# Kernel optimization log

Hardware: AMD Instinct MI355X
Metric: run time of the kernel (lower is better)

The kernel has to match this reference:

```python
import jax, jax.numpy as jnp
import numpy as np

H = 128  # hidden_dim
D = 128  # input_dim


def _lstm_scan(x_seq, Wih, Whh, bih, bhh, reverse=False):
    """x_seq: [T,B,Din]; returns h outputs [T,B,H] in original time order.
    PyTorch LSTMCell gate order: i, f, g, o."""
    hdim = Whh.shape[1]
    B = x_seq.shape[1]
    # Precompute input projections for all timesteps in one GEMM.
    xg = jnp.einsum('tbd,gd->tbg', x_seq, Wih) + bih  # [T,B,4H]

    def step(carry, xg_t):
        h, c = carry
        gates = xg_t + h @ Whh.T + bhh
        i, f, g, o = jnp.split(gates, 4, axis=-1)
        i = jax.nn.sigmoid(i)
        f = jax.nn.sigmoid(f)
        g = jnp.tanh(g)
        o = jax.nn.sigmoid(o)
        c = f * c + i * g
        h = o * jnp.tanh(c)
        return (h, c), h

    h0 = jnp.zeros((B, hdim), dtype=x_seq.dtype)
    c0 = jnp.zeros((B, hdim), dtype=x_seq.dtype)
    _, hs = jax.lax.scan(step, (h0, c0), xg, reverse=reverse)
    return hs  # [T,B,H], original time order (scan reverse handles bw dir)


def _bilstm_layer(x_seq, params_fw, params_bw):
    fw = _lstm_scan(x_seq, *params_fw, reverse=False)
    bw = _lstm_scan(x_seq, *params_bw, reverse=True)
    return jnp.concatenate([fw, bw], axis=-1)  # [T,B,2H]


def _make_cell_params(key, in_dim, hid):
    k1, k2, k3, k4 = jax.random.split(key, 4)
    s = 1.0 / np.sqrt(hid)
    return (
        jax.random.uniform(k1, (4 * hid, in_dim), jnp.float32, -s, s),
        jax.random.uniform(k2, (4 * hid, hid), jnp.float32, -s, s),
        jax.random.uniform(k3, (4 * hid,), jnp.float32, -s, s),
        jax.random.uniform(k4, (4 * hid,), jnp.float32, -s, s),
    )


def setup_inputs() -> dict:
    key = jax.random.key(0)
    ks = jax.random.split(key, 6)
    B, T = 64, 1024
    x = jax.random.normal(ks[0], (B, T, D), jnp.float32)
    lengths = jax.random.randint(ks[1], (B,), 1, T + 1, jnp.int64 if jax.config.jax_enable_x64 else jnp.int32)
    inp = {'x': x, 'lengths': lengths}
    names = ['fw1', 'bw1', 'fw2', 'bw2']
    in_dims = [D, D, 2 * H, 2 * H]
    for name, idim, k in zip(names, in_dims, ks[2:]):
        Wih, Whh, bih, bhh = _make_cell_params(k, idim, H)
        inp[f'Wih_{name}'] = Wih
        inp[f'Whh_{name}'] = Whh
        inp[f'bih_{name}'] = bih
        inp[f'bhh_{name}'] = bhh
    return inp


def reference(x, lengths,
              Wih_fw1, Whh_fw1, bih_fw1, bhh_fw1,
              Wih_bw1, Whh_bw1, bih_bw1, bhh_bw1,
              Wih_fw2, Whh_fw2, bih_fw2, bhh_fw2,
              Wih_bw2, Whh_bw2, bih_bw2, bhh_bw2):
    # lengths is unused in the original forward as well.
    xt = jnp.transpose(x, (1, 0, 2))  # [T,B,D] time-major for scan
    out1 = _bilstm_layer(xt,
                         (Wih_fw1, Whh_fw1, bih_fw1, bhh_fw1),
                         (Wih_bw1, Whh_bw1, bih_bw1, bhh_bw1))
    out2 = _bilstm_layer(out1,
                         (Wih_fw2, Whh_fw2, bih_fw2, bhh_fw2),
                         (Wih_bw2, Whh_bw2, bih_bw2, bhh_bw2))
    return jnp.transpose(out2, (1, 0, 2))  # [B,T,2H]
```

## Files before the change

### kernel.cpp

```cpp
#include <hip/hip_runtime.h>
#include <hip/hip_fp16.h>
#include <stdint.h>


#define T_SEQ 1024
#define B_SZ  64
#define M_TOT 65536

typedef _Float16 h2_t __attribute__((ext_vector_type(2)));
typedef _Float16 f16x8 __attribute__((ext_vector_type(8)));
typedef float f32x4 __attribute__((ext_vector_type(4)));

__device__ inline uint32_t pack2(float a, float b) {
  uint16_t ua = __builtin_bit_cast(uint16_t, (_Float16)a);
  uint16_t ub = __builtin_bit_cast(uint16_t, (_Float16)b);
  return (uint32_t)ua | ((uint32_t)ub << 16);
}

template <int CTRL>
__device__ inline float dppf(float v) {
  return __builtin_bit_cast(
      float, __builtin_amdgcn_update_dpp(0, __builtin_bit_cast(int, v), CTRL,
                                         0xF, 0xF, true));
}


__global__ void prep_whB(const float* __restrict__ Whh, uint32_t* __restrict__ dst) {
  int idx = blockIdx.x * 256 + threadIdx.x;
  int R = idx >> 6, kw = idx & 63;
  int w = R >> 7, nt = (R >> 4) & 7, cc = R & 15;
  int j = 32 * w + 8 * (nt >> 1) + 2 * (cc >> 2) + (nt & 1);
  int g = (cc & 3) * 128 + j;
  dst[idx] = pack2(Whh[g * 128 + 2 * kw], Whh[g * 128 + 2 * kw + 1]);
}

template <int KW>
__global__ void prep_bt(const float* __restrict__ Wih, uint32_t* __restrict__ dst) {
  int idx = blockIdx.x * 256 + threadIdx.x;
  constexpr int SH = (KW == 64) ? 6 : 7;
  int g = idx >> SH, kw = idx & (KW - 1);
  dst[idx] = pack2(Wih[g * (2 * KW) + 2 * kw], Wih[g * (2 * KW) + 2 * kw + 1]);
}

__global__ void prep_biasc(const float* __restrict__ bih, const float* __restrict__ bhh,
                           float* __restrict__ dst) {
  int idx = blockIdx.x * 256 + threadIdx.x;
  if (idx < 512) dst[idx] = bih[idx] + bhh[idx];
}

__global__ void prep_x(const float2* __restrict__ x2, uint32_t* __restrict__ xf16) {
  int idx = blockIdx.x * 256 + threadIdx.x;
  float2 v = x2[idx];
  xf16[idx] = pack2(v.x, v.y);
}

template <int KW>
__global__ __launch_bounds__(256) void xg_gemm(
    const uint32_t* __restrict__ A, const uint32_t* __restrict__ Bt,
    const float* __restrict__ biascat, uint16_t* __restrict__ xg) {
  const int n0 = blockIdx.x * 64;
  const int m0 = blockIdx.y * 64;
  const int tid = threadIdx.x;
  __shared__ uint32_t At[64][36];
  __shared__ uint32_t Bts[64][36];
  const int lr = tid >> 2, lq = tid & 3;
  const int wave = tid >> 6, lane = tid & 63;
  const int wm = wave >> 1, wn = wave & 1;
  const int q = lane >> 4, ln16 = lane & 15;
  f32x4 acc[2][2] = {};
  for (int kb = 0; kb < KW; kb += 16) {
    uint4 av = *(const uint4*)&A[(size_t)(m0 + lr) * KW + kb + lq * 4];
    uint4 bv = *(const uint4*)&Bt[(size_t)(n0 + lr) * KW + kb + lq * 4];
    __syncthreads();
    *(uint4*)&At[lr][lq * 4] = av;
    *(uint4*)&Bts[lr][lq * 4] = bv;
    __syncthreads();
#pragma unroll
    for (int mi = 0; mi < 2; mi++) {
      f16x8 af = *(const f16x8*)&At[wm * 32 + mi * 16 + ln16][q * 4];
#pragma unroll
      for (int ni = 0; ni < 2; ni++) {
        f16x8 bf = *(const f16x8*)&Bts[wn * 32 + ni * 16 + ln16][q * 4];
        acc[mi][ni] = __builtin_amdgcn_mfma_f32_16x16x32_f16(af, bf, acc[mi][ni], 0, 0, 0);
      }
    }
  }
#pragma unroll
  for (int mi = 0; mi < 2; mi++)
#pragma unroll
    for (int ni = 0; ni < 2; ni++) {
      int n = n0 + wn * 32 + ni * 16 + ln16;
      int cell = n >> 9, g = n & 511;
      int j = g & 127, pg = g >> 7;
      int PI = ((j >> 5) << 7) | (((j >> 3) & 3) << 5) | (((j >> 1) & 3) << 3) |
               (pg << 1) | (j & 1);
      float bs = biascat[n];
#pragma unroll
      for (int i = 0; i < 4; i++) {
        int m = m0 + wm * 32 + mi * 16 + q * 4 + i;
        float v = acc[mi][ni][i] + bs;
        xg[((size_t)cell * M_TOT + m) * 512 + PI] =
            __builtin_bit_cast(uint16_t, (_Float16)v);
      }
    }
}

template <bool FINAL>
__global__ __launch_bounds__(256, 1) void scan_kernel(
    const uint16_t* __restrict__ xg, const uint32_t* __restrict__ whB,
    uint32_t* __restrict__ hout, float* __restrict__ fout) {
  const int tid = threadIdx.x;
  const int w = tid >> 6;
  const int lane = tid & 63;
  const int q = lane >> 4;
  const int ln16 = lane & 15;
  const int mq = ln16 >> 2;
  const int p = ln16 & 3;
  const int b = blockIdx.x & 63;
  const int dir = blockIdx.x >> 6;

  __shared__ __align__(16) uint32_t hbuf[2][64];

  f16x8 wb[8][4];
  {
    const uint32_t* wp = whB + (size_t)dir * 512 * 64;
#pragma unroll
    for (int nt = 0; nt < 8; nt++)
#pragma unroll
      for (int kt = 0; kt < 4; kt++)
        wb[nt][kt] = *(const f16x8*)&wp[(128 * w + 16 * nt + ln16) * 64 + 16 * kt + 4 * q];
  }
#pragma unroll
  for (int nt = 0; nt < 8; nt++)
#pragma unroll
    for (int kt = 0; kt < 4; kt++) asm volatile("" : "+v"(wb[nt][kt]));

  const float kmul = (p == 2) ? (-2.0f * 1.44269504f) : -1.44269504f;
  const float gm = (p == 2) ? 2.0f : 1.0f;
  const float gb = (p == 2) ? -1.0f : 0.0f;

  const uint32_t* xgp = (const uint32_t*)xg + ((size_t)dir * M_TOT + (size_t)b * T_SEQ) * 256 + tid;

  if (tid < 64) hbuf[0][tid] = 0u;
  float c0 = 0.0f, c1 = 0.0f;
  const f32x4 zero4 = {0.0f, 0.0f, 0.0f, 0.0f};

  uint32_t xr[8];
#pragma unroll
  for (int k = 0; k < 4; k++) {
    const int tk = dir ? (T_SEQ - 1 - k) : k;
    xr[k] = xgp[(size_t)tk * 256];
  }
  __syncthreads();

  for (int s0 = 0; s0 < T_SEQ; s0 += 8) {
#pragma unroll
    for (int nt = 0; nt < 8; nt++)
#pragma unroll
      for (int kt = 0; kt < 4; kt++) asm volatile("" : "+v"(wb[nt][kt]));
#pragma unroll
    for (int k = 0; k < 8; k++) {
      const int s = s0 + k;
      const int par = k & 1;

      {
        int sn = s + 4;
        sn = (sn < T_SEQ) ? sn : (T_SEQ - 1);
        const int tn = dir ? (T_SEQ - 1 - sn) : sn;
        xr[(k + 4) & 7] = xgp[(size_t)tn * 256];
      }

      const uint4* hb4 = (const uint4*)&hbuf[par][0];
      f32x4 acc[8];
      {
        f16x8 hk = __builtin_bit_cast(f16x8, hb4[q]);
#pragma unroll
        for (int nt = 0; nt < 8; nt++)
          acc[nt] = __builtin_amdgcn_mfma_f32_16x16x32_f16(hk, wb[nt][0], zero4, 0, 0, 0);
      }
#pragma unroll
      for (int kt = 1; kt < 4; kt++) {
        f16x8 hk = __builtin_bit_cast(f16x8, hb4[kt * 4 + q]);
#pragma unroll
        for (int nt = 0; nt < 8; nt++)
          acc[nt] = __builtin_amdgcn_mfma_f32_16x16x32_f16(hk, wb[nt][kt], acc[nt], 0, 0, 0);
      }

      float z0 = (q & 2) ? ((q & 1) ? acc[6][0] : acc[4][0])
                         : ((q & 1) ? acc[2][0] : acc[0][0]);
      float z1 = (q & 2) ? ((q & 1) ? acc[7][0] : acc[5][0])
                         : ((q & 1) ? acc[3][0] : acc[1][0]);

      h2_t xv = __builtin_bit_cast(h2_t, xr[k]);
      z0 += (float)xv[0];
      z1 += (float)xv[1];

      float e0 = __builtin_amdgcn_exp2f(z0 * kmul);
      float e1 = __builtin_amdgcn_exp2f(z1 * kmul);
      float sg0 = __builtin_amdgcn_rcpf(1.0f + e0);
      float sg1 = __builtin_amdgcn_rcpf(1.0f + e1);
      float gv0 = __builtin_fmaf(sg0, gm, gb);
      float gv1 = __builtin_fmaf(sg1, gm, gb);

      float gi0 = dppf<0x00>(gv0), gf0 = dppf<0x55>(gv0);
      float gg0 = dppf<0xAA>(gv0), go0 = dppf<0xFF>(gv0);
      float gi1 = dppf<0x00>(gv1), gf1 = dppf<0x55>(gv1);
      float gg1 = dppf<0xAA>(gv1), go1 = dppf<0xFF>(gv1);

      c0 = __builtin_fmaf(gf0, c0, gi0 * gg0);
      c1 = __builtin_fmaf(gf1, c1, gi1 * gg1);
      float ec0 = __builtin_amdgcn_exp2f(c0 * (-2.0f * 1.44269504f));
      float ec1 = __builtin_amdgcn_exp2f(c1 * (-2.0f * 1.44269504f));
      float th0 = __builtin_fmaf(2.0f, __builtin_amdgcn_rcpf(1.0f + ec0), -1.0f);
      float th1 = __builtin_fmaf(2.0f, __builtin_amdgcn_rcpf(1.0f + ec1), -1.0f);
      float h0 = go0 * th0;
      float h1 = go1 * th1;

      if (p == 0) {
        const int uo = 16 * w + 4 * q + mq;
        uint32_t hu = pack2(h0, h1);
        hbuf[par ^ 1][uo] = hu;
        const int t = dir ? (T_SEQ - 1 - s) : s;
        if (FINAL) {
          float2 hv = {h0, h1};
          ((float2*)fout)[(size_t)(b * T_SEQ + t) * 128 + dir * 64 + uo] = hv;
        } else {
          hout[(size_t)(b * T_SEQ + t) * 128 + dir * 64 + uo] = hu;
        }
      }
      asm volatile("s_waitcnt lgkmcnt(0)" ::: "memory");
      __builtin_amdgcn_s_barrier();
      asm volatile("" ::: "memory");
    }
  }
}

extern "C" void kernel_launch(void* const* d_in, const int* in_sizes, int n_in,
                              void* d_out, int out_size, void* d_ws, size_t ws_size,
                              hipStream_t stream) {
  const float* x = (const float*)d_in[0];
  const float* Wih_fw1 = (const float*)d_in[2];
  const float* Whh_fw1 = (const float*)d_in[3];
  const float* bih_fw1 = (const float*)d_in[4];
  const float* bhh_fw1 = (const float*)d_in[5];
  const float* Wih_bw1 = (const float*)d_in[6];
  const float* Whh_bw1 = (const float*)d_in[7];
  const float* bih_bw1 = (const float*)d_in[8];
  const float* bhh_bw1 = (const float*)d_in[9];
  const float* Wih_fw2 = (const float*)d_in[10];
  const float* Whh_fw2 = (const float*)d_in[11];
  const float* bih_fw2 = (const float*)d_in[12];
  const float* bhh_fw2 = (const float*)d_in[13];
  const float* Wih_bw2 = (const float*)d_in[14];
  const float* Whh_bw2 = (const float*)d_in[15];
  const float* bih_bw2 = (const float*)d_in[16];
  const float* bhh_bw2 = (const float*)d_in[17];

  uint8_t* ws = (uint8_t*)d_ws;
  uint32_t* whbuf = (uint32_t*)(ws + 0);
  uint32_t* btbuf1 = (uint32_t*)(ws + 524288);
  uint32_t* btbuf2 = (uint32_t*)(ws + 786432);
  float* biascat = (float*)(ws + 1310720);
  uint32_t* xf16 = (uint32_t*)(ws + 2097152);
  uint32_t* out1 = (uint32_t*)(ws + 18874368);
  uint16_t* xgbuf = (uint16_t*)(ws + 52428800);
  float* fout = (float*)d_out;

  prep_whB<<<128, 256, 0, stream>>>(Whh_fw1, whbuf + 0 * 32768);
  prep_whB<<<128, 256, 0, stream>>>(Whh_bw1, whbuf + 1 * 32768);
  prep_whB<<<128, 256, 0, stream>>>(Whh_fw2, whbuf + 2 * 32768);
  prep_whB<<<128, 256, 0, stream>>>(Whh_bw2, whbuf + 3 * 32768);
  prep_bt<64><<<128, 256, 0, stream>>>(Wih_fw1, btbuf1 + 0);
  prep_bt<64><<<128, 256, 0, stream>>>(Wih_bw1, btbuf1 + 512 * 64);
  prep_bt<128><<<256, 256, 0, stream>>>(Wih_fw2, btbuf2 + 0);
  prep_bt<128><<<256, 256, 0, stream>>>(Wih_bw2, btbuf2 + 512 * 128);
  prep_biasc<<<2, 256, 0, stream>>>(bih_fw1, bhh_fw1, biascat + 0);
  prep_biasc<<<2, 256, 0, stream>>>(bih_bw1, bhh_bw1, biascat + 512);
  prep_biasc<<<2, 256, 0, stream>>>(bih_fw2, bhh_fw2, biascat + 1024);
  prep_biasc<<<2, 256, 0, stream>>>(bih_bw2, bhh_bw2, biascat + 1536);
  prep_x<<<(B_SZ * T_SEQ * 64) / 256, 256, 0, stream>>>((const float2*)x, xf16);

  xg_gemm<64><<<dim3(16, 1024), 256, 0, stream>>>(xf16, btbuf1, biascat, xgbuf);
  scan_kernel<false><<<128, 256, 0, stream>>>(xgbuf, whbuf + 0, out1, nullptr);

  xg_gemm<128><<<dim3(16, 1024), 256, 0, stream>>>(out1, btbuf2, biascat + 1024, xgbuf);
  scan_kernel<true><<<128, 256, 0, stream>>>(xgbuf, whbuf + 2 * 32768, nullptr, fout);
}
```

Before: 1.327 ms.

## Split recurrent matvec between MFMA and packed dot2 VALU per step

The per-step h·Whh product in the scan kernel is split: half of the hidden units (64) are computed with MFMA as before, and the other half with v_dot2 fp16 instructions from register-resident weights, followed by DPP cross-lane reductions. The aim is to shorten the serial latency of each recurrent step by halving the MFMA chain and running the other half on the VALU at the same time. Weight prep, the xg permutation and the hidden-state layout (now 16-bit per unit, outputs written as two separate halves) are all changed to match. The trade-offs are higher register pressure from 64 extra weight words per thread and extra VALU and DPP work on the critical path.

```diff
diff --git a/kernel.cpp b/kernel.cpp
--- a/kernel.cpp
+++ b/kernel.cpp
@@ -10,6 +10,11 @@
 typedef _Float16 h2_t __attribute__((ext_vector_type(2)));
 typedef _Float16 f16x8 __attribute__((ext_vector_type(8)));
 typedef float f32x4 __attribute__((ext_vector_type(4)));
+
+__device__ inline float dot2(uint32_t a, uint32_t b, float c) {
+  return __builtin_amdgcn_fdot2(__builtin_bit_cast(h2_t, a),
+                                __builtin_bit_cast(h2_t, b), c, false);
+}
 
 __device__ inline uint32_t pack2(float a, float b) {
   uint16_t ua = __builtin_bit_cast(uint16_t, (_Float16)a);
@@ -25,12 +30,18 @@
 }
 
 
-__global__ void prep_whB(const float* __restrict__ Whh, uint32_t* __restrict__ dst) {
+__global__ void prep_whBM(const float* __restrict__ Whh, uint32_t* __restrict__ dst) {
   int idx = blockIdx.x * 256 + threadIdx.x;
   int R = idx >> 6, kw = idx & 63;
-  int w = R >> 7, nt = (R >> 4) & 7, cc = R & 15;
-  int j = 32 * w + 8 * (nt >> 1) + 2 * (cc >> 2) + (nt & 1);
-  int g = (cc & 3) * 128 + j;
+  int w = R >> 6, nt = (R >> 4) & 3, cc = R & 15;
+  int g = (cc & 3) * 128 + 16 * w + 4 * nt + (cc >> 2);
+  dst[idx] = pack2(Whh[g * 128 + 2 * kw], Whh[g * 128 + 2 * kw + 1]);
+}
+
+__global__ void prep_whV(const float* __restrict__ Whh, uint32_t* __restrict__ dst) {
+  int idx = blockIdx.x * 256 + threadIdx.x;
+  int kw = idx >> 8, c2 = idx & 255;
+  int g = (c2 & 3) * 128 + 64 + (c2 >> 2);
   dst[idx] = pack2(Whh[g * 128 + 2 * kw], Whh[g * 128 + 2 * kw + 1]);
 }
 
@@ -92,8 +103,14 @@
       int n = n0 + wn * 32 + ni * 16 + ln16;
       int cell = n >> 9, g = n & 511;
       int j = g & 127, pg = g >> 7;
-      int PI = ((j >> 5) << 7) | (((j >> 3) & 3) << 5) | (((j >> 1) & 3) << 3) |
-               (pg << 1) | (j & 1);
+      int PI;
+      if (j < 64) {
+        int tidm = 64 * (j >> 4) + 16 * ((j >> 2) & 3) + 4 * (j & 3) + pg;
+        PI = tidm << 1;
+      } else {
+        int tidv = 4 * (j - 64) + pg;
+        PI = (tidv << 1) | 1;
+      }
       float bs = biascat[n];
 #pragma unroll
       for (int i = 0; i < 4; i++) {
@@ -107,8 +124,8 @@
 
 template <bool FINAL>
 __global__ __launch_bounds__(256, 1) void scan_kernel(
-    const uint16_t* __restrict__ xg, const uint32_t* __restrict__ whB,
-    uint32_t* __restrict__ hout, float* __restrict__ fout) {
+    const uint16_t* __restrict__ xg, const uint32_t* __restrict__ whc,
+    uint16_t* __restrict__ hout, float* __restrict__ fout) {
   const int tid = threadIdx.x;
   const int w = tid >> 6;
   const int lane = tid & 63;
@@ -116,24 +133,36 @@
   const int ln16 = lane & 15;
   const int mq = ln16 >> 2;
   const int p = ln16 & 3;
+  const int uq = tid >> 2;
   const int b = blockIdx.x & 63;
   const int dir = blockIdx.x >> 6;
 
-  __shared__ __align__(16) uint32_t hbuf[2][64];
-
-  f16x8 wb[8][4];
+  __shared__ __align__(16) uint16_t hbuf[2][128];
+
+  f16x8 wb[4][4];
+  uint32_t wq[4][16];
   {
-    const uint32_t* wp = whB + (size_t)dir * 512 * 64;
-#pragma unroll
-    for (int nt = 0; nt < 8; nt++)
+    const uint32_t* wpm = whc + (size_t)dir * 32768;
+    const uint32_t* wpv = wpm + 16384;
+#pragma unroll
+    for (int nt = 0; nt < 4; nt++)
 #pragma unroll
       for (int kt = 0; kt < 4; kt++)
-        wb[nt][kt] = *(const f16x8*)&wp[(128 * w + 16 * nt + ln16) * 64 + 16 * kt + 4 * q];
+        wb[nt][kt] = *(const f16x8*)&wpm[(64 * w + 16 * nt + ln16) * 64 + 16 * kt + 4 * q];
+#pragma unroll
+    for (int r = 0; r < 4; r++)
+#pragma unroll
+      for (int w2 = 0; w2 < 16; w2++)
+        wq[r][w2] = wpv[(16 * p + w2) * 256 + 4 * uq + r];
   }
 #pragma unroll
-  for (int nt = 0; nt < 8; nt++)
+  for (int nt = 0; nt < 4; nt++)
 #pragma unroll
     for (int kt = 0; kt < 4; kt++) asm volatile("" : "+v"(wb[nt][kt]));
+#pragma unroll
+  for (int r = 0; r < 4; r++)
+#pragma unroll
+    for (int w2 = 0; w2 < 16; w2++) asm volatile("" : "+v"(wq[r][w2]));
 
   const float kmul = (p == 2) ? (-2.0f * 1.44269504f) : -1.44269504f;
   const float gm = (p == 2) ? 2.0f : 1.0f;
@@ -141,7 +170,7 @@
 
   const uint32_t* xgp = (const uint32_t*)xg + ((size_t)dir * M_TOT + (size_t)b * T_SEQ) * 256 + tid;
 
-  if (tid < 64) hbuf[0][tid] = 0u;
+  if (tid < 128) hbuf[0][tid] = (uint16_t)0;
   float c0 = 0.0f, c1 = 0.0f;
   const f32x4 zero4 = {0.0f, 0.0f, 0.0f, 0.0f};
 
@@ -155,9 +184,13 @@
 
   for (int s0 = 0; s0 < T_SEQ; s0 += 8) {
 #pragma unroll
-    for (int nt = 0; nt < 8; nt++)
+    for (int nt = 0; nt < 4; nt++)
 #pragma unroll
       for (int kt = 0; kt < 4; kt++) asm volatile("" : "+v"(wb[nt][kt]));
+#pragma unroll
+    for (int r = 0; r < 4; r++)
+#pragma unroll
+      for (int w2 = 0; w2 < 16; w2++) asm volatile("" : "+v"(wq[r][w2]));
 #pragma unroll
     for (int k = 0; k < 8; k++) {
       const int s = s0 + k;
@@ -171,29 +204,59 @@
       }
 
       const uint4* hb4 = (const uint4*)&hbuf[par][0];
-      f32x4 acc[8];
+      f32x4 acc[4];
       {
         f16x8 hk = __builtin_bit_cast(f16x8, hb4[q]);
 #pragma unroll
-        for (int nt = 0; nt < 8; nt++)
+        for (int nt = 0; nt < 4; nt++)
           acc[nt] = __builtin_amdgcn_mfma_f32_16x16x32_f16(hk, wb[nt][0], zero4, 0, 0, 0);
       }
 #pragma unroll
       for (int kt = 1; kt < 4; kt++) {
         f16x8 hk = __builtin_bit_cast(f16x8, hb4[kt * 4 + q]);
 #pragma unroll
-        for (int nt = 0; nt < 8; nt++)
+        for (int nt = 0; nt < 4; nt++)
           acc[nt] = __builtin_amdgcn_mfma_f32_16x16x32_f16(hk, wb[nt][kt], acc[nt], 0, 0, 0);
       }
 
-      float z0 = (q & 2) ? ((q & 1) ? acc[6][0] : acc[4][0])
-                         : ((q & 1) ? acc[2][0] : acc[0][0]);
-      float z1 = (q & 2) ? ((q & 1) ? acc[7][0] : acc[5][0])
-                         : ((q & 1) ? acc[3][0] : acc[1][0]);
+      float a0 = 0.f, a1 = 0.f, a2 = 0.f, a3 = 0.f;
+      const uint4* ib = (const uint4*)(&hbuf[par][p * 32]);
+#pragma unroll
+      for (int kk = 0; kk < 4; kk++) {
+        uint4 v = ib[kk];
+        a0 = dot2(v.x, wq[0][4 * kk + 0], a0);
+        a1 = dot2(v.x, wq[1][4 * kk + 0], a1);
+        a2 = dot2(v.x, wq[2][4 * kk + 0], a2);
+        a3 = dot2(v.x, wq[3][4 * kk + 0], a3);
+        a0 = dot2(v.y, wq[0][4 * kk + 1], a0);
+        a1 = dot2(v.y, wq[1][4 * kk + 1], a1);
+        a2 = dot2(v.y, wq[2][4 * kk + 1], a2);
+        a3 = dot2(v.y, wq[3][4 * kk + 1], a3);
+        a0 = dot2(v.z, wq[0][4 * kk + 2], a0);
+        a1 = dot2(v.z, wq[1][4 * kk + 2], a1);
+        a2 = dot2(v.z, wq[2][4 * kk + 2], a2);
+        a3 = dot2(v.z, wq[3][4 * kk + 2], a3);
+        a0 = dot2(v.w, wq[0][4 * kk + 3], a0);
+        a1 = dot2(v.w, wq[1][4 * kk + 3], a1);
+        a2 = dot2(v.w, wq[2][4 * kk + 3], a2);
+        a3 = dot2(v.w, wq[3][4 * kk + 3], a3);
+      }
+      float keep1 = (p & 1) ? a1 : a0;
+      float send1 = (p & 1) ? a0 : a1;
+      float u = keep1 + dppf<0xB1>(send1);
+      float keep2 = (p & 1) ? a3 : a2;
+      float send2 = (p & 1) ? a2 : a3;
+      float v2 = keep2 + dppf<0xB1>(send2);
+      float keep3 = (p & 2) ? v2 : u;
+      float send3 = (p & 2) ? u : v2;
+      float zv = keep3 + dppf<0x4E>(send3);
+
+      float zm = (q & 2) ? ((q & 1) ? acc[3][0] : acc[2][0])
+                         : ((q & 1) ? acc[1][0] : acc[0][0]);
 
       h2_t xv = __builtin_bit_cast(h2_t, xr[k]);
-      z0 += (float)xv[0];
-      z1 += (float)xv[1];
+      float z0 = zm + (float)xv[0];
+      float z1 = zv + (float)xv[1];
 
       float e0 = __builtin_amdgcn_exp2f(z0 * kmul);
       float e1 = __builtin_amdgcn_exp2f(z1 * kmul);
@@ -217,15 +280,19 @@
       float h1 = go1 * th1;
 
       if (p == 0) {
-        const int uo = 16 * w + 4 * q + mq;
-        uint32_t hu = pack2(h0, h1);
-        hbuf[par ^ 1][uo] = hu;
+        const int u0 = 16 * w + 4 * q + mq;
+        uint16_t hu0 = __builtin_bit_cast(uint16_t, (_Float16)h0);
+        uint16_t hu1 = __builtin_bit_cast(uint16_t, (_Float16)h1);
+        hbuf[par ^ 1][u0] = hu0;
+        hbuf[par ^ 1][u0 + 64] = hu1;
         const int t = dir ? (T_SEQ - 1 - s) : s;
+        const size_t ob = (size_t)(b * T_SEQ + t) * 256 + dir * 128 + u0;
         if (FINAL) {
-          float2 hv = {h0, h1};
-          ((float2*)fout)[(size_t)(b * T_SEQ + t) * 128 + dir * 64 + uo] = hv;
+          fout[ob] = h0;
+          fout[ob + 64] = h1;
         } else {
-          hout[(size_t)(b * T_SEQ + t) * 128 + dir * 64 + uo] = hu;
+          hout[ob] = hu0;
+          hout[ob + 64] = hu1;
         }
       }
       asm volatile("s_waitcnt lgkmcnt(0)" ::: "memory");
@@ -262,14 +329,18 @@
   uint32_t* btbuf2 = (uint32_t*)(ws + 786432);
   float* biascat = (float*)(ws + 1310720);
   uint32_t* xf16 = (uint32_t*)(ws + 2097152);
-  uint32_t* out1 = (uint32_t*)(ws + 18874368);
+  uint16_t* out1 = (uint16_t*)(ws + 18874368);
   uint16_t* xgbuf = (uint16_t*)(ws + 52428800);
   float* fout = (float*)d_out;
 
-  prep_whB<<<128, 256, 0, stream>>>(Whh_fw1, whbuf + 0 * 32768);
-  prep_whB<<<128, 256, 0, stream>>>(Whh_bw1, whbuf + 1 * 32768);
-  prep_whB<<<128, 256, 0, stream>>>(Whh_fw2, whbuf + 2 * 32768);
-  prep_whB<<<128, 256, 0, stream>>>(Whh_bw2, whbuf + 3 * 32768);
+  prep_whBM<<<64, 256, 0, stream>>>(Whh_fw1, whbuf + 0 * 32768);
+  prep_whV<<<64, 256, 0, stream>>>(Whh_fw1, whbuf + 0 * 32768 + 16384);
+  prep_whBM<<<64, 256, 0, stream>>>(Whh_bw1, whbuf + 1 * 32768);
+  prep_whV<<<64, 256, 0, stream>>>(Whh_bw1, whbuf + 1 * 32768 + 16384);
+  prep_whBM<<<64, 256, 0, stream>>>(Whh_fw2, whbuf + 2 * 32768);
+  prep_whV<<<64, 256, 0, stream>>>(Whh_fw2, whbuf + 2 * 32768 + 16384);
+  prep_whBM<<<64, 256, 0, stream>>>(Whh_bw2, whbuf + 3 * 32768);
+  prep_whV<<<64, 256, 0, stream>>>(Whh_bw2, whbuf + 3 * 32768 + 16384);
   prep_bt<64><<<128, 256, 0, stream>>>(Wih_fw1, btbuf1 + 0);
   prep_bt<64><<<128, 256, 0, stream>>>(Wih_bw1, btbuf1 + 512 * 64);
   prep_bt<128><<<256, 256, 0, stream>>>(Wih_fw2, btbuf2 + 0);
@@ -283,6 +354,6 @@
   xg_gemm<64><<<dim3(16, 1024), 256, 0, stream>>>(xf16, btbuf1, biascat, xgbuf);
   scan_kernel<false><<<128, 256, 0, stream>>>(xgbuf, whbuf + 0, out1, nullptr);
 
-  xg_gemm<128><<<dim3(16, 1024), 256, 0, stream>>>(out1, btbuf2, biascat + 1024, xgbuf);
+  xg_gemm<128><<<dim3(16, 1024), 256, 0, stream>>>((const uint32_t*)out1, btbuf2, biascat + 1024, xgbuf);
   scan_kernel<true><<<128, 256, 0, stream>>>(xgbuf, whbuf + 2 * 32768, nullptr, fout);
 }
```

Result: slower. 1.661 ms (+25.2%).
